# Optimization experiments

Measured on AMD Instinct MI355X. Metric: run time of the kernel, lower is better.

Reference implementation:

```python
import jax, jax.numpy as jnp
import numpy as np

B, H = 2048, 1024
P_DROP = 0.6


def setup_inputs() -> dict:
    key = jax.random.key(0)
    ks = jax.random.split(key, 17)
    stdv = 1.0 / np.sqrt(H)
    u = lambda k, shape: jax.random.uniform(k, shape, jnp.float32, -stdv, stdv)
    inp = {
        'input': jax.random.normal(ks[0], (B, H), jnp.float32),
        'hidden': jax.random.normal(ks[1], (B, H), jnp.float32),
        'pre_cell': jax.random.normal(ks[2], (B, H), jnp.float32),
        # weights are (hidden_size, input_size) and used as input @ W (requires H == input_size)
        'w_i': u(ks[3], (H, H)), 'w_f': u(ks[4], (H, H)),
        'w_o': u(ks[5], (H, H)), 'w_c': u(ks[6], (H, H)),
        'u_i': u(ks[7], (H, H)), 'u_f': u(ks[8], (H, H)),
        'u_o': u(ks[9], (H, H)), 'u_c': u(ks[10], (H, H)),
        'bias1': u(ks[11], (H,)), 'bias2': u(ks[12], (H,)),
        'bias3': u(ks[13], (H,)), 'bias4': u(ks[14], (H,)),
    }
    # F.dropout(training=True) mask, pre-scaled by 1/(1-p); shape matches h_t [B,1,H]
    keep = jax.random.bernoulli(ks[15], 1.0 - P_DROP, (B, 1, H))
    inp['drop_mask'] = keep.astype(jnp.float32) / (1.0 - P_DROP)
    return inp


def reference(input, hidden, pre_cell, w_i, w_f, w_o, w_c, u_i, u_f, u_o, u_c,
              bias1, bias2, bias3, bias4, drop_mask):
    # Fuse the 8 small GEMMs into 2 big ones: gate order (f, i, o, c)
    Wx = jnp.concatenate([w_f, w_i, w_o, w_c], axis=1)   # [H, 4H]
    Wh = jnp.concatenate([u_f, u_i, u_o, u_c], axis=1)   # [H, 4H]
    b = jnp.concatenate([bias1, bias2, bias3, bias4])    # [4H]
    gates = input @ Wx + hidden @ Wh + b                 # [B, 4H]
    f_t, i_t, o_t, g_t = jnp.split(gates, 4, axis=1)
    f_t = jax.nn.sigmoid(f_t)
    i_t = jax.nn.sigmoid(i_t)
    o_t = jax.nn.sigmoid(o_t)
    g_t = jnp.tanh(g_t)
    c_t = pre_cell * f_t + i_t * g_t                     # [B, H]
    h_t = o_t * jnp.tanh(c_t)                            # [B, H]
    h_t = h_t[:, None, :] * drop_mask                    # dropout (training=True)
    c_t = c_t[:, None, :]
    return h_t, c_t
```

## Files before the change

kernel.cpp:

```cpp
#include <hip/hip_runtime.h>
#include <hip/hip_bf16.h>
#include <cstdint>

#define B_DIM 2048
#define H_DIM 1024
#define K_DIM 2048
#define N_DIM 4096

typedef unsigned short u16;
typedef __attribute__((ext_vector_type(8))) short bf16x8;
typedef __attribute__((ext_vector_type(8))) unsigned short u16x8;
typedef __attribute__((ext_vector_type(4))) float f32x4;

__device__ __forceinline__ u16 f2bf(float f) {
    unsigned int u = __float_as_uint(f);
    u += 0x7FFFu + ((u >> 16) & 1u);
    return (u16)(u >> 16);
}

__device__ __forceinline__ float sigmoid_f(float x) {
    return 1.0f / (1.0f + __expf(-x));
}

__device__ __forceinline__ float tanh_f(float x) {
    float e = __expf(2.0f * x);
    return 1.0f - 2.0f / (e + 1.0f);
}

__device__ __forceinline__ void async16(const u16* g, u16* l) {
    __builtin_amdgcn_global_load_lds(
        (const __attribute__((address_space(1))) unsigned int*)g,
        (__attribute__((address_space(3))) unsigned int*)l,
        16, 0, 0);
}

__global__ __launch_bounds__(256) void pack_A(const float* __restrict__ input,
                                              const float* __restrict__ hidden,
                                              u16* __restrict__ A) {
    int idx = (blockIdx.x * 256 + threadIdx.x) * 4;
    int m = idx >> 11;
    int k = idx & (K_DIM - 1);
    const float* src = (k < H_DIM) ? (input + (size_t)m * H_DIM + k)
                                   : (hidden + (size_t)m * H_DIM + (k - H_DIM));
    float4 v = *(const float4*)src;
    ushort4 o;
    o.x = f2bf(v.x); o.y = f2bf(v.y); o.z = f2bf(v.z); o.w = f2bf(v.w);
    *(ushort4*)(A + idx) = o;
}

__global__ __launch_bounds__(256) void pack_B(
    const float* __restrict__ w_f, const float* __restrict__ w_i,
    const float* __restrict__ w_o, const float* __restrict__ w_c,
    const float* __restrict__ u_f, const float* __restrict__ u_i,
    const float* __restrict__ u_o, const float* __restrict__ u_c,
    u16* __restrict__ Bt) {
    __shared__ float tile[32][65];
    const int z = blockIdx.z;
    const float* M;
    switch (z) {
        case 0: M = w_f; break;
        case 1: M = w_i; break;
        case 2: M = w_o; break;
        case 3: M = w_c; break;
        case 4: M = u_f; break;
        case 5: M = u_i; break;
        case 6: M = u_o; break;
        default: M = u_c; break;
    }
    const int g = z & 3;
    const int half = z >> 2;
    const int h0 = blockIdx.x * 32;
    const int k0 = blockIdx.y * 64;
    const int t = threadIdx.x;
#pragma unroll
    for (int it = 0; it < 2; it++) {
        int kl = (t >> 3) + it * 32;
        int hl = (t & 7) * 4;
        float4 v = *(const float4*)(M + (size_t)(k0 + kl) * H_DIM + h0 + hl);
        tile[hl + 0][kl] = v.x;
        tile[hl + 1][kl] = v.y;
        tile[hl + 2][kl] = v.z;
        tile[hl + 3][kl] = v.w;
    }
    __syncthreads();
    {
        int hl = t >> 3;
        int ko = (t & 7) * 8;
        u16x8 o;
#pragma unroll
        for (int q = 0; q < 8; q++) o[q] = f2bf(tile[hl][ko + q]);
        size_t n = 4 * (size_t)(h0 + hl) + g;
        *(u16x8*)(Bt + n * K_DIM + half * H_DIM + k0 + ko) = o;
    }
}

__global__ __launch_bounds__(256) void pack_bias(
    const float* __restrict__ b1, const float* __restrict__ b2,
    const float* __restrict__ b3, const float* __restrict__ b4,
    float* __restrict__ bias_il) {
    int idx = blockIdx.x * 256 + threadIdx.x;
    int h = idx >> 2, g = idx & 3;
    const float* b = (g == 0) ? b1 : (g == 1) ? b2 : (g == 2) ? b3 : b4;
    bias_il[idx] = b[h];
}

#define BM 128
#define BN 128
#define BK 32

__global__ __launch_bounds__(256, 2) void gemm_fused(
    const u16* __restrict__ A, const u16* __restrict__ Bt,
    const float* __restrict__ bias_il, const float* __restrict__ pre_cell,
    const float* __restrict__ mask, float* __restrict__ out) {
    __shared__ char smem[17408];
    u16* As = (u16*)smem;
    u16* Bs = (u16*)(smem + 8192);
    float* et = (float*)smem;

    const int t = threadIdx.x;
    const int w = t >> 6, l = t & 63;
    const int m0 = blockIdx.y * BM;
    const int n0 = blockIdx.x * BN;
    const int wr = w >> 1;
    const int wc = w & 1;
    const int lrow = l & 15;
    const int quad = l >> 4;

    const int sr = w * 16 + (l >> 2);
    const int sc = (l & 3) * 8;
    const u16* Ag0 = A + (size_t)(m0 + sr) * K_DIM + sc;
    const u16* Ag1 = Ag0 + (size_t)64 * K_DIM;
    const u16* Bg0 = Bt + (size_t)(n0 + sr) * K_DIM + sc;
    const u16* Bg1 = Bg0 + (size_t)64 * K_DIM;
    u16* Al0 = As + sr * BK + sc;
    u16* Al1 = Al0 + 64 * BK;
    u16* Bl0 = Bs + sr * BK + sc;
    u16* Bl1 = Bl0 + 64 * BK;

    const u16* afr = As + (wr * 64 + lrow) * BK + quad * 8;
    const u16* bfr = Bs + (wc * 64 + lrow) * BK + quad * 8;

    f32x4 acc[4][4];
#pragma unroll
    for (int j = 0; j < 4; j++) {
        float bv = bias_il[n0 + wc * 64 + j * 16 + lrow];
#pragma unroll
        for (int i = 0; i < 4; i++) acc[i][j] = (f32x4){bv, bv, bv, bv};
    }

    for (int k0 = 0; k0 < K_DIM; k0 += BK) {
        __syncthreads();
        async16(Ag0 + k0, Al0);
        async16(Ag1 + k0, Al1);
        async16(Bg0 + k0, Bl0);
        async16(Bg1 + k0, Bl1);
        __syncthreads();
        bf16x8 af[4], bf[4];
#pragma unroll
        for (int i = 0; i < 4; i++) af[i] = *(const bf16x8*)(afr + i * 16 * BK);
#pragma unroll
        for (int j = 0; j < 4; j++) bf[j] = *(const bf16x8*)(bfr + j * 16 * BK);
#pragma unroll
        for (int i = 0; i < 4; i++)
#pragma unroll
            for (int j = 0; j < 4; j++)
                acc[i][j] = __builtin_amdgcn_mfma_f32_16x16x32_bf16(
                    af[i], bf[j], acc[i][j], 0, 0, 0);
    }

    const int row = t >> 1;
    const int half = t & 1;
    const size_t orow = (size_t)(m0 + row) * H_DIM;
#pragma unroll
    for (int j = 0; j < 4; j++) {
        __syncthreads();
#pragma unroll
        for (int i = 0; i < 4; i++)
#pragma unroll
            for (int r = 0; r < 4; r++)
                et[(wr * 64 + i * 16 + quad * 4 + r) * 33 + wc * 16 + lrow] =
                    acc[i][j][r];
        __syncthreads();
        const int hg0 = (n0 >> 2) + half * 16 + j * 4;
        const float* ep = et + row * 33 + half * 16;
        float4 pc = *(const float4*)(pre_cell + orow + hg0);
        float4 mk = *(const float4*)(mask + orow + hg0);
        const float* ppc = (const float*)&pc;
        const float* pmk = (const float*)&mk;
        float4 oh, oc;
        float* poh = (float*)&oh;
        float* poc = (float*)&oc;
#pragma unroll
        for (int q = 0; q < 4; q++) {
            float fv = sigmoid_f(ep[4 * q + 0]);
            float iv = sigmoid_f(ep[4 * q + 1]);
            float ov = sigmoid_f(ep[4 * q + 2]);
            float gv = tanh_f(ep[4 * q + 3]);
            float cv = ppc[q] * fv + iv * gv;
            poc[q] = cv;
            poh[q] = ov * tanh_f(cv) * pmk[q];
        }
        *(float4*)(out + orow + hg0) = oh;
        *(float4*)(out + (size_t)B_DIM * H_DIM + orow + hg0) = oc;
    }
}

extern "C" void kernel_launch(void* const* d_in, const int* in_sizes, int n_in,
                              void* d_out, int out_size, void* d_ws, size_t ws_size,
                              hipStream_t stream) {
    const float* input    = (const float*)d_in[0];
    const float* hidden   = (const float*)d_in[1];
    const float* pre_cell = (const float*)d_in[2];
    const float* w_i = (const float*)d_in[3];
    const float* w_f = (const float*)d_in[4];
    const float* w_o = (const float*)d_in[5];
    const float* w_c = (const float*)d_in[6];
    const float* u_i = (const float*)d_in[7];
    const float* u_f = (const float*)d_in[8];
    const float* u_o = (const float*)d_in[9];
    const float* u_c = (const float*)d_in[10];
    const float* b1  = (const float*)d_in[11];
    const float* b2  = (const float*)d_in[12];
    const float* b3  = (const float*)d_in[13];
    const float* b4  = (const float*)d_in[14];
    const float* mask = (const float*)d_in[15];
    float* out = (float*)d_out;

    char* ws = (char*)d_ws;
    u16*   A       = (u16*)ws;
    u16*   Bt      = (u16*)(ws + (size_t)8 * 1024 * 1024);
    float* bias_il = (float*)(ws + (size_t)24 * 1024 * 1024);

    pack_A<<<dim3((B_DIM * K_DIM) / (256 * 4)), dim3(256), 0, stream>>>(input, hidden, A);
    pack_B<<<dim3(32, 16, 8), dim3(256), 0, stream>>>(w_f, w_i, w_o, w_c,
                                                      u_f, u_i, u_o, u_c, Bt);
    pack_bias<<<dim3(16), dim3(256), 0, stream>>>(b1, b2, b3, b4, bias_il);
    gemm_fused<<<dim3(N_DIM / BN, B_DIM / BM), dim3(256), 0, stream>>>(
        A, Bt, bias_il, pre_cell, mask, out);
}
```

Baseline: 179.5 us.

## Halve GEMM N-tile for occupancy and merge pack kernels into one launch

Shrinks the GEMM tile to 128x64 with launch bounds of 4 blocks per CU, doubling grid size, and stages the full accumulator tile in LDS for a single-pass epilogue. Merges the three packing kernels into one launch to cut launch overhead. The smaller tile lowers MFMA work per A-tile load, raising global/LDS traffic per flop, and the epilogue buffer raises LDS per block.

```diff
diff --git a/kernel.cpp b/kernel.cpp
--- a/kernel.cpp
+++ b/kernel.cpp
@@ -34,56 +34,61 @@
         16, 0, 0);
 }
 
-__global__ __launch_bounds__(256) void pack_A(const float* __restrict__ input,
-                                              const float* __restrict__ hidden,
-                                              u16* __restrict__ A) {
-    int idx = (blockIdx.x * 256 + threadIdx.x) * 4;
-    int m = idx >> 11;
-    int k = idx & (K_DIM - 1);
-    const float* src = (k < H_DIM) ? (input + (size_t)m * H_DIM + k)
-                                   : (hidden + (size_t)m * H_DIM + (k - H_DIM));
-    float4 v = *(const float4*)src;
-    ushort4 o;
-    o.x = f2bf(v.x); o.y = f2bf(v.y); o.z = f2bf(v.z); o.w = f2bf(v.w);
-    *(ushort4*)(A + idx) = o;
-}
-
-__global__ __launch_bounds__(256) void pack_B(
+__global__ __launch_bounds__(256) void pack_all(
+    const float* __restrict__ input, const float* __restrict__ hidden,
     const float* __restrict__ w_f, const float* __restrict__ w_i,
     const float* __restrict__ w_o, const float* __restrict__ w_c,
     const float* __restrict__ u_f, const float* __restrict__ u_i,
     const float* __restrict__ u_o, const float* __restrict__ u_c,
-    u16* __restrict__ Bt) {
+    const float* __restrict__ b1, const float* __restrict__ b2,
+    const float* __restrict__ b3, const float* __restrict__ b4,
+    u16* __restrict__ A, u16* __restrict__ Bt, float* __restrict__ bias_il) {
     __shared__ float tile[32][65];
-    const int z = blockIdx.z;
-    const float* M;
-    switch (z) {
-        case 0: M = w_f; break;
-        case 1: M = w_i; break;
-        case 2: M = w_o; break;
-        case 3: M = w_c; break;
-        case 4: M = u_f; break;
-        case 5: M = u_i; break;
-        case 6: M = u_o; break;
-        default: M = u_c; break;
-    }
-    const int g = z & 3;
-    const int half = z >> 2;
-    const int h0 = blockIdx.x * 32;
-    const int k0 = blockIdx.y * 64;
+    const int blk = blockIdx.x;
     const int t = threadIdx.x;
-#pragma unroll
-    for (int it = 0; it < 2; it++) {
-        int kl = (t >> 3) + it * 32;
-        int hl = (t & 7) * 4;
-        float4 v = *(const float4*)(M + (size_t)(k0 + kl) * H_DIM + h0 + hl);
-        tile[hl + 0][kl] = v.x;
-        tile[hl + 1][kl] = v.y;
-        tile[hl + 2][kl] = v.z;
-        tile[hl + 3][kl] = v.w;
-    }
-    __syncthreads();
-    {
+
+    if (blk < 4096) {
+        int idx = (blk * 256 + t) * 4;
+        int m = idx >> 11;
+        int k = idx & (K_DIM - 1);
+        const float* src = (k < H_DIM) ? (input + (size_t)m * H_DIM + k)
+                                       : (hidden + (size_t)m * H_DIM + (k - H_DIM));
+        float4 v = *(const float4*)src;
+        ushort4 o;
+        o.x = f2bf(v.x); o.y = f2bf(v.y); o.z = f2bf(v.z); o.w = f2bf(v.w);
+        *(ushort4*)(A + idx) = o;
+    } else if (blk < 8192) {
+        int b2i = blk - 4096;
+        int z = b2i >> 9;
+        int rem = b2i & 511;
+        int hx = rem & 31;
+        int ky = rem >> 5;
+        const float* M;
+        switch (z) {
+            case 0: M = w_f; break;
+            case 1: M = w_i; break;
+            case 2: M = w_o; break;
+            case 3: M = w_c; break;
+            case 4: M = u_f; break;
+            case 5: M = u_i; break;
+            case 6: M = u_o; break;
+            default: M = u_c; break;
+        }
+        const int g = z & 3;
+        const int half = z >> 2;
+        const int h0 = hx * 32;
+        const int k0 = ky * 64;
+#pragma unroll
+        for (int it = 0; it < 2; it++) {
+            int kl = (t >> 3) + it * 32;
+            int hl = (t & 7) * 4;
+            float4 v = *(const float4*)(M + (size_t)(k0 + kl) * H_DIM + h0 + hl);
+            tile[hl + 0][kl] = v.x;
+            tile[hl + 1][kl] = v.y;
+            tile[hl + 2][kl] = v.z;
+            tile[hl + 3][kl] = v.w;
+        }
+        __syncthreads();
         int hl = t >> 3;
         int ko = (t & 7) * 8;
         u16x8 o;
@@ -91,28 +96,24 @@
         for (int q = 0; q < 8; q++) o[q] = f2bf(tile[hl][ko + q]);
         size_t n = 4 * (size_t)(h0 + hl) + g;
         *(u16x8*)(Bt + n * K_DIM + half * H_DIM + k0 + ko) = o;
-    }
-}
-
-__global__ __launch_bounds__(256) void pack_bias(
-    const float* __restrict__ b1, const float* __restrict__ b2,
-    const float* __restrict__ b3, const float* __restrict__ b4,
-    float* __restrict__ bias_il) {
-    int idx = blockIdx.x * 256 + threadIdx.x;
-    int h = idx >> 2, g = idx & 3;
-    const float* b = (g == 0) ? b1 : (g == 1) ? b2 : (g == 2) ? b3 : b4;
-    bias_il[idx] = b[h];
+    } else {
+        int idx = (blk - 8192) * 256 + t;
+        int h = idx >> 2, g = idx & 3;
+        const float* b = (g == 0) ? b1 : (g == 1) ? b2 : (g == 2) ? b3 : b4;
+        bias_il[idx] = b[h];
+    }
 }
 
 #define BM 128
-#define BN 128
+#define BN 64
 #define BK 32
-
-__global__ __launch_bounds__(256, 2) void gemm_fused(
+#define ES 65
+
+__global__ __launch_bounds__(256, 4) void gemm_fused(
     const u16* __restrict__ A, const u16* __restrict__ Bt,
     const float* __restrict__ bias_il, const float* __restrict__ pre_cell,
     const float* __restrict__ mask, float* __restrict__ out) {
-    __shared__ char smem[17408];
+    __shared__ char smem[BM * ES * 4];
     u16* As = (u16*)smem;
     u16* Bs = (u16*)(smem + 8192);
     float* et = (float*)smem;
@@ -131,19 +132,17 @@
     const u16* Ag0 = A + (size_t)(m0 + sr) * K_DIM + sc;
     const u16* Ag1 = Ag0 + (size_t)64 * K_DIM;
     const u16* Bg0 = Bt + (size_t)(n0 + sr) * K_DIM + sc;
-    const u16* Bg1 = Bg0 + (size_t)64 * K_DIM;
     u16* Al0 = As + sr * BK + sc;
     u16* Al1 = Al0 + 64 * BK;
     u16* Bl0 = Bs + sr * BK + sc;
-    u16* Bl1 = Bl0 + 64 * BK;
 
     const u16* afr = As + (wr * 64 + lrow) * BK + quad * 8;
-    const u16* bfr = Bs + (wc * 64 + lrow) * BK + quad * 8;
-
-    f32x4 acc[4][4];
-#pragma unroll
-    for (int j = 0; j < 4; j++) {
-        float bv = bias_il[n0 + wc * 64 + j * 16 + lrow];
+    const u16* bfr = Bs + (wc * 32 + lrow) * BK + quad * 8;
+
+    f32x4 acc[4][2];
+#pragma unroll
+    for (int j = 0; j < 2; j++) {
+        float bv = bias_il[n0 + wc * 32 + j * 16 + lrow];
 #pragma unroll
         for (int i = 0; i < 4; i++) acc[i][j] = (f32x4){bv, bv, bv, bv};
     }
@@ -153,55 +152,77 @@
         async16(Ag0 + k0, Al0);
         async16(Ag1 + k0, Al1);
         async16(Bg0 + k0, Bl0);
-        async16(Bg1 + k0, Bl1);
         __syncthreads();
-        bf16x8 af[4], bf[4];
+        bf16x8 af[4], bf[2];
 #pragma unroll
         for (int i = 0; i < 4; i++) af[i] = *(const bf16x8*)(afr + i * 16 * BK);
 #pragma unroll
-        for (int j = 0; j < 4; j++) bf[j] = *(const bf16x8*)(bfr + j * 16 * BK);
+        for (int j = 0; j < 2; j++) bf[j] = *(const bf16x8*)(bfr + j * 16 * BK);
 #pragma unroll
         for (int i = 0; i < 4; i++)
 #pragma unroll
-            for (int j = 0; j < 4; j++)
+            for (int j = 0; j < 2; j++)
                 acc[i][j] = __builtin_amdgcn_mfma_f32_16x16x32_bf16(
                     af[i], bf[j], acc[i][j], 0, 0, 0);
     }
 
-    const int row = t >> 1;
-    const int half = t & 1;
-    const size_t orow = (size_t)(m0 + row) * H_DIM;
-#pragma unroll
-    for (int j = 0; j < 4; j++) {
-        __syncthreads();
-#pragma unroll
-        for (int i = 0; i < 4; i++)
+    __syncthreads();
+#pragma unroll
+    for (int i = 0; i < 4; i++)
+#pragma unroll
+        for (int j = 0; j < 2; j++) {
+            int r0 = wr * 64 + i * 16 + quad * 4;
+            int c0 = wc * 32 + j * 16 + lrow;
 #pragma unroll
             for (int r = 0; r < 4; r++)
-                et[(wr * 64 + i * 16 + quad * 4 + r) * 33 + wc * 16 + lrow] =
-                    acc[i][j][r];
-        __syncthreads();
-        const int hg0 = (n0 >> 2) + half * 16 + j * 4;
-        const float* ep = et + row * 33 + half * 16;
-        float4 pc = *(const float4*)(pre_cell + orow + hg0);
-        float4 mk = *(const float4*)(mask + orow + hg0);
-        const float* ppc = (const float*)&pc;
-        const float* pmk = (const float*)&mk;
-        float4 oh, oc;
-        float* poh = (float*)&oh;
-        float* poc = (float*)&oc;
+                et[(r0 + r) * ES + c0] = acc[i][j][r];
+        }
+    __syncthreads();
+    {
+        const int row = t >> 1;
+        const int halfh = t & 1;
+        const int hb0 = (n0 >> 2) + halfh * 8;
+        const size_t orow = (size_t)(m0 + row) * H_DIM + hb0;
+        const float* ep = et + row * ES + halfh * 32;
+        float4 pc0 = *(const float4*)(pre_cell + orow);
+        float4 pc1 = *(const float4*)(pre_cell + orow + 4);
+        float4 mk0 = *(const float4*)(mask + orow);
+        float4 mk1 = *(const float4*)(mask + orow + 4);
+        const float* ppc0 = (const float*)&pc0;
+        const float* ppc1 = (const float*)&pc1;
+        const float* pmk0 = (const float*)&mk0;
+        const float* pmk1 = (const float*)&mk1;
+        float4 oh0, oh1, oc0, oc1;
+        float* poh0 = (float*)&oh0;
+        float* poh1 = (float*)&oh1;
+        float* poc0 = (float*)&oc0;
+        float* poc1 = (float*)&oc1;
 #pragma unroll
         for (int q = 0; q < 4; q++) {
             float fv = sigmoid_f(ep[4 * q + 0]);
             float iv = sigmoid_f(ep[4 * q + 1]);
             float ov = sigmoid_f(ep[4 * q + 2]);
             float gv = tanh_f(ep[4 * q + 3]);
-            float cv = ppc[q] * fv + iv * gv;
-            poc[q] = cv;
-            poh[q] = ov * tanh_f(cv) * pmk[q];
-        }
-        *(float4*)(out + orow + hg0) = oh;
-        *(float4*)(out + (size_t)B_DIM * H_DIM + orow + hg0) = oc;
+            float cv = ppc0[q] * fv + iv * gv;
+            poc0[q] = cv;
+            poh0[q] = ov * tanh_f(cv) * pmk0[q];
+        }
+#pragma unroll
+        for (int q = 0; q < 4; q++) {
+            float fv = sigmoid_f(ep[16 + 4 * q + 0]);
+            float iv = sigmoid_f(ep[16 + 4 * q + 1]);
+            float ov = sigmoid_f(ep[16 + 4 * q + 2]);
+            float gv = tanh_f(ep[16 + 4 * q + 3]);
+            float cv = ppc1[q] * fv + iv * gv;
+            poc1[q] = cv;
+            poh1[q] = ov * tanh_f(cv) * pmk1[q];
+        }
+        float* outh = out + orow;
+        float* outc = out + (size_t)B_DIM * H_DIM + orow;
+        *(float4*)(outh) = oh0;
+        *(float4*)(outh + 4) = oh1;
+        *(float4*)(outc) = oc0;
+        *(float4*)(outc + 4) = oc1;
     }
 }
 
@@ -231,10 +252,9 @@
     u16*   Bt      = (u16*)(ws + (size_t)8 * 1024 * 1024);
     float* bias_il = (float*)(ws + (size_t)24 * 1024 * 1024);
 
-    pack_A<<<dim3((B_DIM * K_DIM) / (256 * 4)), dim3(256), 0, stream>>>(input, hidden, A);
-    pack_B<<<dim3(32, 16, 8), dim3(256), 0, stream>>>(w_f, w_i, w_o, w_c,
-                                                      u_f, u_i, u_o, u_c, Bt);
-    pack_bias<<<dim3(16), dim3(256), 0, stream>>>(b1, b2, b3, b4, bias_il);
+    pack_all<<<dim3(4096 + 4096 + 16), dim3(256), 0, stream>>>(
+        input, hidden, w_f, w_i, w_o, w_c, u_f, u_i, u_o, u_c,
+        b1, b2, b3, b4, A, Bt, bias_il);
     gemm_fused<<<dim3(N_DIM / BN, B_DIM / BM), dim3(256), 0, stream>>>(
         A, Bt, bias_il, pre_cell, mask, out);
 }
```

Measured after the change: 185.7 us. 1.03x slower.

## Merge pack kernels into one launch, double BK to 64, prefetch epilogue loads

Applied to the files above, without the earlier changes.

Folds the three packing kernels (activations, transposed weights, bias) into a single launch that dispatches on block index, which removes two kernel launches and their gaps. The GEMM's K-step grows from 32 to 64 by loading two 32-wide LDS sub-tiles per iteration, so the number of barrier pairs in the main loop is halved. The pre_cell and dropout-mask loads in the epilogue are moved ahead of the LDS transpose loop so their latency overlaps it. In exchange, LDS per block grows to 32KB and the epilogue holds more registers, which may limit occupancy.

```diff
diff --git a/kernel.cpp b/kernel.cpp
--- a/kernel.cpp
+++ b/kernel.cpp
@@ -34,56 +34,61 @@
         16, 0, 0);
 }
 
-__global__ __launch_bounds__(256) void pack_A(const float* __restrict__ input,
-                                              const float* __restrict__ hidden,
-                                              u16* __restrict__ A) {
-    int idx = (blockIdx.x * 256 + threadIdx.x) * 4;
-    int m = idx >> 11;
-    int k = idx & (K_DIM - 1);
-    const float* src = (k < H_DIM) ? (input + (size_t)m * H_DIM + k)
-                                   : (hidden + (size_t)m * H_DIM + (k - H_DIM));
-    float4 v = *(const float4*)src;
-    ushort4 o;
-    o.x = f2bf(v.x); o.y = f2bf(v.y); o.z = f2bf(v.z); o.w = f2bf(v.w);
-    *(ushort4*)(A + idx) = o;
-}
-
-__global__ __launch_bounds__(256) void pack_B(
+__global__ __launch_bounds__(256) void pack_all(
+    const float* __restrict__ input, const float* __restrict__ hidden,
     const float* __restrict__ w_f, const float* __restrict__ w_i,
     const float* __restrict__ w_o, const float* __restrict__ w_c,
     const float* __restrict__ u_f, const float* __restrict__ u_i,
     const float* __restrict__ u_o, const float* __restrict__ u_c,
-    u16* __restrict__ Bt) {
+    const float* __restrict__ b1, const float* __restrict__ b2,
+    const float* __restrict__ b3, const float* __restrict__ b4,
+    u16* __restrict__ A, u16* __restrict__ Bt, float* __restrict__ bias_il) {
     __shared__ float tile[32][65];
-    const int z = blockIdx.z;
-    const float* M;
-    switch (z) {
-        case 0: M = w_f; break;
-        case 1: M = w_i; break;
-        case 2: M = w_o; break;
-        case 3: M = w_c; break;
-        case 4: M = u_f; break;
-        case 5: M = u_i; break;
-        case 6: M = u_o; break;
-        default: M = u_c; break;
-    }
-    const int g = z & 3;
-    const int half = z >> 2;
-    const int h0 = blockIdx.x * 32;
-    const int k0 = blockIdx.y * 64;
+    const int blk = blockIdx.x;
     const int t = threadIdx.x;
-#pragma unroll
-    for (int it = 0; it < 2; it++) {
-        int kl = (t >> 3) + it * 32;
-        int hl = (t & 7) * 4;
-        float4 v = *(const float4*)(M + (size_t)(k0 + kl) * H_DIM + h0 + hl);
-        tile[hl + 0][kl] = v.x;
-        tile[hl + 1][kl] = v.y;
-        tile[hl + 2][kl] = v.z;
-        tile[hl + 3][kl] = v.w;
-    }
-    __syncthreads();
-    {
+
+    if (blk < 4096) {
+        int idx = (blk * 256 + t) * 4;
+        int m = idx >> 11;
+        int k = idx & (K_DIM - 1);
+        const float* src = (k < H_DIM) ? (input + (size_t)m * H_DIM + k)
+                                       : (hidden + (size_t)m * H_DIM + (k - H_DIM));
+        float4 v = *(const float4*)src;
+        ushort4 o;
+        o.x = f2bf(v.x); o.y = f2bf(v.y); o.z = f2bf(v.z); o.w = f2bf(v.w);
+        *(ushort4*)(A + idx) = o;
+    } else if (blk < 8192) {
+        int b2i = blk - 4096;
+        int z = b2i >> 9;
+        int rem = b2i & 511;
+        int hx = rem & 31;
+        int ky = rem >> 5;
+        const float* M;
+        switch (z) {
+            case 0: M = w_f; break;
+            case 1: M = w_i; break;
+            case 2: M = w_o; break;
+            case 3: M = w_c; break;
+            case 4: M = u_f; break;
+            case 5: M = u_i; break;
+            case 6: M = u_o; break;
+            default: M = u_c; break;
+        }
+        const int g = z & 3;
+        const int half = z >> 2;
+        const int h0 = hx * 32;
+        const int k0 = ky * 64;
+#pragma unroll
+        for (int it = 0; it < 2; it++) {
+            int kl = (t >> 3) + it * 32;
+            int hl = (t & 7) * 4;
+            float4 v = *(const float4*)(M + (size_t)(k0 + kl) * H_DIM + h0 + hl);
+            tile[hl + 0][kl] = v.x;
+            tile[hl + 1][kl] = v.y;
+            tile[hl + 2][kl] = v.z;
+            tile[hl + 3][kl] = v.w;
+        }
+        __syncthreads();
         int hl = t >> 3;
         int ko = (t & 7) * 8;
         u16x8 o;
@@ -91,30 +96,28 @@
         for (int q = 0; q < 8; q++) o[q] = f2bf(tile[hl][ko + q]);
         size_t n = 4 * (size_t)(h0 + hl) + g;
         *(u16x8*)(Bt + n * K_DIM + half * H_DIM + k0 + ko) = o;
-    }
-}
-
-__global__ __launch_bounds__(256) void pack_bias(
-    const float* __restrict__ b1, const float* __restrict__ b2,
-    const float* __restrict__ b3, const float* __restrict__ b4,
-    float* __restrict__ bias_il) {
-    int idx = blockIdx.x * 256 + threadIdx.x;
-    int h = idx >> 2, g = idx & 3;
-    const float* b = (g == 0) ? b1 : (g == 1) ? b2 : (g == 2) ? b3 : b4;
-    bias_il[idx] = b[h];
+    } else {
+        int idx = (blk - 8192) * 256 + t;
+        int h = idx >> 2, g = idx & 3;
+        const float* b = (g == 0) ? b1 : (g == 1) ? b2 : (g == 2) ? b3 : b4;
+        bias_il[idx] = b[h];
+    }
 }
 
 #define BM 128
 #define BN 128
-#define BK 32
+#define BK 64
+#define SL (64 * 32)
 
 __global__ __launch_bounds__(256, 2) void gemm_fused(
     const u16* __restrict__ A, const u16* __restrict__ Bt,
     const float* __restrict__ bias_il, const float* __restrict__ pre_cell,
     const float* __restrict__ mask, float* __restrict__ out) {
-    __shared__ char smem[17408];
-    u16* As = (u16*)smem;
-    u16* Bs = (u16*)(smem + 8192);
+    __shared__ char smem[32768];
+    u16* AsL = (u16*)smem;
+    u16* AsH = (u16*)(smem + 8192);
+    u16* BsL = (u16*)(smem + 16384);
+    u16* BsH = (u16*)(smem + 24576);
     float* et = (float*)smem;
 
     const int t = threadIdx.x;
@@ -132,13 +135,10 @@
     const u16* Ag1 = Ag0 + (size_t)64 * K_DIM;
     const u16* Bg0 = Bt + (size_t)(n0 + sr) * K_DIM + sc;
     const u16* Bg1 = Bg0 + (size_t)64 * K_DIM;
-    u16* Al0 = As + sr * BK + sc;
-    u16* Al1 = Al0 + 64 * BK;
-    u16* Bl0 = Bs + sr * BK + sc;
-    u16* Bl1 = Bl0 + 64 * BK;
-
-    const u16* afr = As + (wr * 64 + lrow) * BK + quad * 8;
-    const u16* bfr = Bs + (wc * 64 + lrow) * BK + quad * 8;
+    const int soff = sr * 32 + sc;
+
+    const int foA = (wr * 64 + lrow) * 32 + quad * 8;
+    const int foB = (wc * 64 + lrow) * 32 + quad * 8;
 
     f32x4 acc[4][4];
 #pragma unroll
@@ -148,29 +148,47 @@
         for (int i = 0; i < 4; i++) acc[i][j] = (f32x4){bv, bv, bv, bv};
     }
 
+#define COMPUTE(Asb, Bsb)                                                   \
+    {                                                                       \
+        bf16x8 af[4], bf[4];                                                \
+        _Pragma("unroll") for (int i = 0; i < 4; i++)                       \
+            af[i] = *(const bf16x8*)(Asb + foA + i * 16 * 32);              \
+        _Pragma("unroll") for (int j = 0; j < 4; j++)                       \
+            bf[j] = *(const bf16x8*)(Bsb + foB + j * 16 * 32);              \
+        _Pragma("unroll") for (int i = 0; i < 4; i++)                       \
+            _Pragma("unroll") for (int j = 0; j < 4; j++)                   \
+                acc[i][j] = __builtin_amdgcn_mfma_f32_16x16x32_bf16(        \
+                    af[i], bf[j], acc[i][j], 0, 0, 0);                      \
+    }
+
     for (int k0 = 0; k0 < K_DIM; k0 += BK) {
         __syncthreads();
-        async16(Ag0 + k0, Al0);
-        async16(Ag1 + k0, Al1);
-        async16(Bg0 + k0, Bl0);
-        async16(Bg1 + k0, Bl1);
-        __syncthreads();
-        bf16x8 af[4], bf[4];
-#pragma unroll
-        for (int i = 0; i < 4; i++) af[i] = *(const bf16x8*)(afr + i * 16 * BK);
-#pragma unroll
-        for (int j = 0; j < 4; j++) bf[j] = *(const bf16x8*)(bfr + j * 16 * BK);
-#pragma unroll
-        for (int i = 0; i < 4; i++)
-#pragma unroll
-            for (int j = 0; j < 4; j++)
-                acc[i][j] = __builtin_amdgcn_mfma_f32_16x16x32_bf16(
-                    af[i], bf[j], acc[i][j], 0, 0, 0);
-    }
+        async16(Ag0 + k0, AsL + soff);
+        async16(Ag1 + k0, AsL + soff + SL);
+        async16(Ag0 + k0 + 32, AsH + soff);
+        async16(Ag1 + k0 + 32, AsH + soff + SL);
+        async16(Bg0 + k0, BsL + soff);
+        async16(Bg1 + k0, BsL + soff + SL);
+        async16(Bg0 + k0 + 32, BsH + soff);
+        async16(Bg1 + k0 + 32, BsH + soff + SL);
+        __syncthreads();
+        COMPUTE(AsL, BsL);
+        COMPUTE(AsH, BsH);
+    }
+#undef COMPUTE
 
     const int row = t >> 1;
     const int half = t & 1;
     const size_t orow = (size_t)(m0 + row) * H_DIM;
+
+    float4 pc[4], mk[4];
+#pragma unroll
+    for (int j = 0; j < 4; j++) {
+        const int hg0 = (n0 >> 2) + half * 16 + j * 4;
+        pc[j] = *(const float4*)(pre_cell + orow + hg0);
+        mk[j] = *(const float4*)(mask + orow + hg0);
+    }
+
 #pragma unroll
     for (int j = 0; j < 4; j++) {
         __syncthreads();
@@ -183,10 +201,8 @@
         __syncthreads();
         const int hg0 = (n0 >> 2) + half * 16 + j * 4;
         const float* ep = et + row * 33 + half * 16;
-        float4 pc = *(const float4*)(pre_cell + orow + hg0);
-        float4 mk = *(const float4*)(mask + orow + hg0);
-        const float* ppc = (const float*)&pc;
-        const float* pmk = (const float*)&mk;
+        const float* ppc = (const float*)&pc[j];
+        const float* pmk = (const float*)&mk[j];
         float4 oh, oc;
         float* poh = (float*)&oh;
         float* poc = (float*)&oc;
@@ -231,10 +247,9 @@
     u16*   Bt      = (u16*)(ws + (size_t)8 * 1024 * 1024);
     float* bias_il = (float*)(ws + (size_t)24 * 1024 * 1024);
 
-    pack_A<<<dim3((B_DIM * K_DIM) / (256 * 4)), dim3(256), 0, stream>>>(input, hidden, A);
-    pack_B<<<dim3(32, 16, 8), dim3(256), 0, stream>>>(w_f, w_i, w_o, w_c,
-                                                      u_f, u_i, u_o, u_c, Bt);
-    pack_bias<<<dim3(16), dim3(256), 0, stream>>>(b1, b2, b3, b4, bias_il);
+    pack_all<<<dim3(4096 + 4096 + 16), dim3(256), 0, stream>>>(
+        input, hidden, w_f, w_i, w_o, w_c, u_f, u_i, u_o, u_c,
+        b1, b2, b3, b4, A, Bt, bias_il);
     gemm_fused<<<dim3(N_DIM / BN, B_DIM / BM), dim3(256), 0, stream>>>(
         A, Bt, bias_il, pre_cell, mask, out);
 }
```

New measurement: 168.9 us. 5.9% less time.
